# Kernel optimization log

Hardware: AMD Instinct MI355X
Metric: run time of the kernel (lower is better)

Reference implementation:

```python
import jax, jax.numpy as jnp
import numpy as np

RES = 16            # voxel grid resolution (init arg res)
G = RES ** 3        # number of cells = 4096
REG_R = float(np.sqrt(3.0)) / RES  # sqrt(3)/s regularizer radius
B, C, RND, NPTS, H = 16, 64, 2, 16384, 256


def _grid_offsets():
    # util.meshgrid(res): integer grid coords, then ((grid+0.5)/res - 0.5).view(3,-1)
    r = jnp.arange(RES)
    gx, gy, gz = jnp.meshgrid(r, r, r, indexing='ij')
    grid = jnp.stack([gx, gy, gz], 0).reshape(3, -1).astype(jnp.float32)  # [3, G]
    return (grid + 0.5) / RES - 0.5


def _dens_sample(dens, n_points):
    # Deterministic largest-remainder allocation of n_points proportional to density.
    b = dens.shape[0]
    p = dens.reshape(b, -1)
    p = p / jnp.sum(p, axis=-1, keepdims=True)
    scaled = p * n_points                      # [b, G]
    base = jnp.floor(scaled)
    rem = (n_points - jnp.sum(base, axis=-1)).astype(jnp.int32)   # [b]
    frac = scaled - base
    ranks = jnp.argsort(jnp.argsort(-frac, axis=-1), axis=-1)      # rank by fractional part
    return base.astype(jnp.int32) + (ranks < rem[:, None]).astype(jnp.int32)  # [b, G]


def setup_inputs() -> dict:
    key = jax.random.key(0)
    ks = jax.random.split(key, 9)
    cin = C + RND
    f32 = jnp.float32
    return {
        'x': jax.random.normal(ks[0], (B, C, RES, RES, RES), f32),
        'dens': jax.random.uniform(ks[1], (B, RES, RES, RES), f32) + 1e-3,
        'noise': jax.random.uniform(ks[2], (B, RND, NPTS), f32),
        'W1': jax.random.normal(ks[3], (H, cin), f32) * np.float32(1.0 / np.sqrt(cin)),
        'b1': jnp.zeros((H,), f32),
        'W2': jax.random.normal(ks[4], (H, H), f32) * np.float32(1.0 / np.sqrt(H)),
        'b2': jnp.zeros((H,), f32),
        'W3': jax.random.normal(ks[5], (3, H), f32) * np.float32(1.0 / np.sqrt(H)),
        'b3': jnp.zeros((3,), f32),
        'n_points': NPTS,
    }


def reference(x, dens, noise, W1, b1, W2, b2, W3, b3, n_points):
    b, c = x.shape[0], x.shape[1]
    x_flat = x.reshape(b, c, -1)                        # [b, c, G]
    n = _dens_sample(dens, n_points)                    # [b, G] repeat counts, sums to n_points
    # Vectorized replacement for the nonzero()/cat loop: cell i appears n[i] times.
    cell_ids = jnp.arange(G)
    idx = jax.vmap(lambda ni: jnp.repeat(cell_ids, ni, total_repeat_length=n_points))(n)  # [b, n_points]
    x_ind = jnp.take_along_axis(x_flat, idx[:, None, :], axis=2)   # [b, c, n_points]
    o = _grid_offsets()                                 # [3, G]
    gen_off = jnp.transpose(o[:, idx], (1, 0, 2))       # [b, 3, n_points]
    rnd = noise * 2.0 - 1.0                             # uniform in [-1, 1)
    gen_inp = jnp.concatenate([x_ind, rnd], axis=1)     # [b, c+rnd, n_points]
    # pointwise conv1d MLP generator
    h = jax.nn.relu(jnp.einsum('oc,bcn->bon', W1, gen_inp) + b1[:, None])
    h = jax.nn.relu(jnp.einsum('oh,bhn->bon', W2, h) + b2[:, None])
    out = jnp.einsum('oh,bhn->bon', W3, h) + b3[:, None]            # [b, 3, n_points]
    norm = jnp.sqrt(jnp.sum(out * out, axis=1))                      # [b, n_points]
    reg = jnp.maximum(norm - REG_R, 0.0)
    return (out + gen_off, reg)
```

## Files before the change

### kernel.cpp

```cpp
#include <hip/hip_runtime.h>

typedef unsigned long long u64;
typedef _Float16 f16x8 __attribute__((ext_vector_type(8)));
typedef float    f32x4 __attribute__((ext_vector_type(4)));
typedef __fp16   fp16x2 __attribute__((ext_vector_type(2)));

#define G_    4096
#define NPTS  16384

union H8 { _Float16 h[8]; uint4 u; };
union PK2 { fp16x2 h[2]; uint2 u; };
union PK4 { fp16x2 h[4]; uint4 u; };

#define MFMA_(A_,B_,C_) __builtin_amdgcn_mfma_f32_16x16x32_f16((A_),(B_),(C_),0,0,0)


__global__ __launch_bounds__(256) void kP(const float* __restrict__ dens,
                                          int* __restrict__ pc,
                                          const float* __restrict__ W1,
                                          const float* __restrict__ W2,
                                          const float* __restrict__ W3,
                                          _Float16* __restrict__ w1f,
                                          _Float16* __restrict__ w2f,
                                          _Float16* __restrict__ w3f,
                                          float* __restrict__ w1n){
  __shared__ double sred[256];
  __shared__ u64  keys[4096];
  __shared__ int  nvs[4096];
  __shared__ int  binidx[4096];
  __shared__ int  hist[1024];
  __shared__ int  cab[1024];
  __shared__ int  scan[256];
  __shared__ float Sf;
  __shared__ int  remS, BstarS, needS, cntS;
  const int t = threadIdx.x;

  if (blockIdx.x >= 16){
    const int e = (blockIdx.x - 16)*256 + t;
    H8 v;
    if (e < 8192){
      const int RT = e >> 9, kt = (e >> 6) & 7, l = e & 63;
      const int m = RT*16 + (l & 15), k = kt*32 + ((l >> 4) << 3);
      #pragma unroll
      for (int j = 0; j < 8; ++j) v.h[j] = (_Float16)W2[m*256 + k + j];
      *(uint4*)&w2f[e*8] = v.u;
    } else if (e < 10240){
      const int e2 = e - 8192;
      const int RT = e2 >> 7, r2 = e2 & 127, kt = r2 >> 6, l = r2 & 63;
      const int m = RT*16 + (l & 15), k = kt*32 + ((l >> 4) << 3);
      #pragma unroll
      for (int j = 0; j < 8; ++j) v.h[j] = (_Float16)W1[m*66 + k + j];
      *(uint4*)&w1f[e2*8] = v.u;
    } else if (e < 10752){
      const int e3 = e - 10240;
      const int kt = e3 >> 6, l = e3 & 63;
      const int m = l & 15, k = kt*32 + ((l >> 4) << 3);
      #pragma unroll
      for (int j = 0; j < 8; ++j) v.h[j] = (m < 3) ? (_Float16)W3[m*256 + k + j] : (_Float16)0.f;
      *(uint4*)&w3f[e3*8] = v.u;
    } else if (e < 11008){
      const int r = e - 10752;
      w1n[r*2 + 0] = W1[r*66 + 64];
      w1n[r*2 + 1] = W1[r*66 + 65];
    }
    return;
  }

  const int b = blockIdx.x;
  const float* d = dens + b*G_;

  for (int j = t; j < 1024; j += 256) hist[j] = 0;
  if (t == 0) cntS = 0;

  double s = 0.0;
  for (int j = 0; j < 16; ++j) s += (double)d[t + 256*j];
  sred[t] = s; __syncthreads();
  for (int off = 128; off > 0; off >>= 1){
    if (t < off) sred[t] += sred[t + off];
    __syncthreads();
  }
  if (t == 0) Sf = (float)sred[0];
  __syncthreads();
  const float S = Sf;

  int bi[16]; int bs = 0;
  #pragma unroll
  for (int j = 0; j < 16; ++j){
    const int i = t + 256*j;
    const float p  = d[i] / S;
    const float sc = p * 16384.0f;
    const float fl = floorf(sc);
    const float fr = sc - fl;
    bi[j] = (int)fl; bs += bi[j];
    const unsigned fb = __float_as_uint(fr);
    keys[i] = ((u64)fb << 12) | (u64)(4095 - i);
    atomicAdd(&hist[fb >> 20], 1);
  }
  scan[t] = bs; __syncthreads();
  for (int off = 128; off > 0; off >>= 1){
    if (t < off) scan[t] += scan[t + off];
    __syncthreads();
  }
  if (t == 0) remS = 16384 - scan[0];
  __syncthreads();
  const int rem = remS;

  const int h0 = hist[4*t], h1 = hist[4*t+1], h2 = hist[4*t+2], h3 = hist[4*t+3];
  const int gs = h0 + h1 + h2 + h3;
  __syncthreads();
  scan[t] = gs; __syncthreads();
  for (int off = 1; off < 256; off <<= 1){
    const int v2 = (t + off < 256) ? scan[t + off] : 0;
    __syncthreads();
    scan[t] += v2;
    __syncthreads();
  }
  const int sAfter = scan[t] - gs;
  cab[4*t+3] = sAfter;
  cab[4*t+2] = sAfter + h3;
  cab[4*t+1] = sAfter + h3 + h2;
  cab[4*t+0] = sAfter + h3 + h2 + h1;
  if (t == 0){ BstarS = 0x7fffffff; needS = 0; }
  __syncthreads();
  if (rem > 0){
    const int ca[4] = {cab[4*t], cab[4*t+1], cab[4*t+2], cab[4*t+3]};
    const int hh[4] = {h0, h1, h2, h3};
    #pragma unroll
    for (int q = 0; q < 4; ++q)
      if (ca[q] < rem && rem <= ca[q] + hh[q]){ BstarS = 4*t + q; needS = rem - ca[q]; }
  }
  __syncthreads();
  const int Bstar = BstarS, need = needS;

  #pragma unroll
  for (int j = 0; j < 16; ++j){
    const int i = t + 256*j;
    const int bin = (int)(keys[i] >> 32);
    nvs[i] = bi[j] + ((bin > Bstar) ? 1 : 0);
    if (bin == Bstar){ const int pos = atomicAdd(&cntS, 1); binidx[pos] = i; }
  }
  __syncthreads();
  const int cnt = cntS;
  for (int p = t; p < cnt; p += 256){
    const u64 K = keys[binidx[p]];
    int r = 0;
    for (int q = 0; q < cnt; ++q) r += (keys[binidx[q]] > K) ? 1 : 0;
    if (r < need) nvs[binidx[p]] += 1;
  }
  __syncthreads();

  int loc[16]; int ls = 0;
  #pragma unroll
  for (int j = 0; j < 16; ++j){ loc[j] = nvs[t*16 + j]; ls += loc[j]; }
  __syncthreads();
  scan[t] = ls; __syncthreads();
  for (int off = 1; off < 256; off <<= 1){
    const int v2 = (t >= off) ? scan[t - off] : 0;
    __syncthreads();
    scan[t] += v2;
    __syncthreads();
  }
  int off0 = scan[t] - ls;
  int* o = pc + b*NPTS;
  #pragma unroll
  for (int j = 0; j < 16; ++j){
    const int c = t*16 + j;
    for (int r = 0; r < loc[j]; ++r) o[off0++] = c;
  }
}

__global__ __launch_bounds__(256, 3) void kE(
    const float* __restrict__ x, const float* __restrict__ noise,
    const _Float16* __restrict__ w1f, const _Float16* __restrict__ w2f,
    const _Float16* __restrict__ w3f, const float* __restrict__ w1n,
    const float* __restrict__ b1, const float* __restrict__ b2, const float* __restrict__ b3,
    const int* __restrict__ pc, float* __restrict__ out)
{
  __shared__ _Float16 Hb[16384];
  __shared__ int   cells[64];
  __shared__ float rndS[2][64];
  const int b = blockIdx.y, p0 = blockIdx.x*64, tid = threadIdx.x;
  const int w = tid >> 6, lane = tid & 63;

  const int pt_g  = tid >> 2;
  const int cell_g = pc[b*NPTS + p0 + pt_g];
  if (tid < 64) cells[tid] = pc[b*NPTS + p0 + tid];
  if (tid >= 64 && tid < 192){
    const int rr = (tid - 64) >> 6, p = tid & 63;
    rndS[rr][p] = noise[(b*2 + rr)*NPTS + p0 + p]*2.f - 1.f;
  }
  {
    const int koct = tid & 3;
    const int ct = pt_g >> 4, lane2 = (pt_g & 15) + koct*16;
    #pragma unroll
    for (int kt = 0; kt < 2; ++kt){
      const int kbase = kt*32 + koct*8;
      const float* xb = x + ((size_t)(b*64 + kbase))*G_ + cell_g;
      float xv[8];
      #pragma unroll
      for (int j = 0; j < 8; ++j) xv[j] = xb[(size_t)j*G_];
      PK4 v;
      v.h[0] = __builtin_amdgcn_cvt_pkrtz(xv[0], xv[1]);
      v.h[1] = __builtin_amdgcn_cvt_pkrtz(xv[2], xv[3]);
      v.h[2] = __builtin_amdgcn_cvt_pkrtz(xv[4], xv[5]);
      v.h[3] = __builtin_amdgcn_cvt_pkrtz(xv[6], xv[7]);
      *(uint4*)&Hb[((kt*4 + ct)*64 + lane2)*8] = v.u;
    }
  }
  __syncthreads();

  f32x4 acc[4][4];
  const f32x4 zz = {0.f, 0.f, 0.f, 0.f};
  #pragma unroll
  for (int rt = 0; rt < 4; ++rt)
    #pragma unroll
    for (int ct = 0; ct < 4; ++ct) acc[rt][ct] = zz;

  const int wr = w*4;

  __builtin_amdgcn_s_setprio(1);
  #pragma unroll
  for (int kt = 0; kt < 2; ++kt){
    f16x8 B[4];
    #pragma unroll
    for (int ct = 0; ct < 4; ++ct) B[ct] = *(f16x8*)&Hb[((kt*4 + ct)*64 + lane)*8];
    #pragma unroll
    for (int rt = 0; rt < 4; ++rt){
      f16x8 A = *(const f16x8*)&w1f[(((wr + rt)*2 + kt)*64 + lane)*8];
      #pragma unroll
      for (int ct = 0; ct < 4; ++ct)
        acc[rt][ct] = MFMA_(A, B[ct], acc[rt][ct]);
    }
  }
  __builtin_amdgcn_s_setprio(0);

  f16x8 A0[4], A1[4];
  #pragma unroll
  for (int rt = 0; rt < 4; ++rt){
    A0[rt] = *(const f16x8*)&w2f[(((wr + rt)*8 + 0)*64 + lane)*8];
    A1[rt] = *(const f16x8*)&w2f[(((wr + rt)*8 + 1)*64 + lane)*8];
  }

  {
    const int m16 = lane & 15, khi = lane >> 4;
    float rn0[4], rn1[4];
    #pragma unroll
    for (int ct = 0; ct < 4; ++ct){
      rn0[ct] = rndS[0][ct*16 + m16];
      rn1[ct] = rndS[1][ct*16 + m16];
    }
    #pragma unroll
    for (int rt = 0; rt < 4; ++rt){
      const int row0 = w*64 + rt*16 + khi*4;
      const float4 wa = *(const float4*)&w1n[row0*2];
      const float4 wb = *(const float4*)&w1n[row0*2 + 4];
      #pragma unroll
      for (int ct = 0; ct < 4; ++ct){
        acc[rt][ct][0] += wa.x*rn0[ct] + wa.y*rn1[ct];
        acc[rt][ct][1] += wa.z*rn0[ct] + wa.w*rn1[ct];
        acc[rt][ct][2] += wb.x*rn0[ct] + wb.y*rn1[ct];
        acc[rt][ct][3] += wb.z*rn0[ct] + wb.w*rn1[ct];
      }
    }
  }
  __syncthreads();

  #pragma unroll
  for (int rt = 0; rt < 4; ++rt){
    const int row0 = w*64 + rt*16 + ((lane >> 4) << 2);
    const float4 bq = *(const float4*)&b1[row0];
    const int kt2 = row0 >> 5, c16 = (row0 >> 3) & 3, j0 = row0 & 7;
    const int lane2 = (lane & 15) + c16*16;
    #pragma unroll
    for (int ct = 0; ct < 4; ++ct){
      PK2 v;
      v.h[0] = __builtin_amdgcn_cvt_pkrtz(fmaxf(acc[rt][ct][0] + bq.x, 0.f),
                                          fmaxf(acc[rt][ct][1] + bq.y, 0.f));
      v.h[1] = __builtin_amdgcn_cvt_pkrtz(fmaxf(acc[rt][ct][2] + bq.z, 0.f),
                                          fmaxf(acc[rt][ct][3] + bq.w, 0.f));
      *(uint2*)&Hb[((kt2*4 + ct)*64 + lane2)*8 + j0] = v.u;
      acc[rt][ct] = zz;
    }
  }
  __syncthreads();

  __builtin_amdgcn_s_setprio(1);
#define MFMA4(AR, RT) \
    acc[RT][0] = MFMA_(AR, Bv0, acc[RT][0]); \
    acc[RT][1] = MFMA_(AR, Bv1, acc[RT][1]); \
    acc[RT][2] = MFMA_(AR, Bv2, acc[RT][2]); \
    acc[RT][3] = MFMA_(AR, Bv3, acc[RT][3]);
#define L2STEP(KT, ACUR) { \
    f16x8 Bv0 = *(f16x8*)&Hb[(((KT)*4 + 0)*64 + lane)*8]; \
    f16x8 Bv1 = *(f16x8*)&Hb[(((KT)*4 + 1)*64 + lane)*8]; \
    f16x8 Bv2 = *(f16x8*)&Hb[(((KT)*4 + 2)*64 + lane)*8]; \
    f16x8 Bv3 = *(f16x8*)&Hb[(((KT)*4 + 3)*64 + lane)*8]; \
    MFMA4(ACUR[0], 0); \
    if ((KT) + 2 < 8) ACUR[0] = *(const f16x8*)&w2f[(((wr + 0)*8 + (KT) + 2)*64 + lane)*8]; \
    MFMA4(ACUR[1], 1); \
    if ((KT) + 2 < 8) ACUR[1] = *(const f16x8*)&w2f[(((wr + 1)*8 + (KT) + 2)*64 + lane)*8]; \
    MFMA4(ACUR[2], 2); \
    if ((KT) + 2 < 8) ACUR[2] = *(const f16x8*)&w2f[(((wr + 2)*8 + (KT) + 2)*64 + lane)*8]; \
    MFMA4(ACUR[3], 3); \
    if ((KT) + 2 < 8) ACUR[3] = *(const f16x8*)&w2f[(((wr + 3)*8 + (KT) + 2)*64 + lane)*8]; \
  }
  L2STEP(0, A0)
  L2STEP(1, A1)
  L2STEP(2, A0)
  L2STEP(3, A1)
  L2STEP(4, A0)
  L2STEP(5, A1)
  L2STEP(6, A0)
  L2STEP(7, A1)
#undef L2STEP
#undef MFMA4
  __builtin_amdgcn_s_setprio(0);

  f16x8 W3v[8];
  #pragma unroll
  for (int kt = 0; kt < 8; ++kt) W3v[kt] = *(const f16x8*)&w3f[(kt*64 + lane)*8];
  __syncthreads();

  #pragma unroll
  for (int rt = 0; rt < 4; ++rt){
    const int row0 = w*64 + rt*16 + ((lane >> 4) << 2);
    const float4 bq = *(const float4*)&b2[row0];
    const int kt2 = row0 >> 5, c16 = (row0 >> 3) & 3, j0 = row0 & 7;
    const int lane2 = (lane & 15) + c16*16;
    #pragma unroll
    for (int ct = 0; ct < 4; ++ct){
      PK2 v;
      v.h[0] = __builtin_amdgcn_cvt_pkrtz(fmaxf(acc[rt][ct][0] + bq.x, 0.f),
                                          fmaxf(acc[rt][ct][1] + bq.y, 0.f));
      v.h[1] = __builtin_amdgcn_cvt_pkrtz(fmaxf(acc[rt][ct][2] + bq.z, 0.f),
                                          fmaxf(acc[rt][ct][3] + bq.w, 0.f));
      *(uint2*)&Hb[((kt2*4 + ct)*64 + lane2)*8 + j0] = v.u;
    }
  }
  __syncthreads();

  f32x4 a3 = zz;
  __builtin_amdgcn_s_setprio(1);
  #pragma unroll
  for (int kt = 0; kt < 8; ++kt){
    f16x8 B = *(f16x8*)&Hb[((kt*4 + w)*64 + lane)*8];
    a3 = MFMA_(W3v[kt], B, a3);
  }
  __builtin_amdgcn_s_setprio(0);
  if (lane < 16){
    const float ox = a3[0] + b3[0];
    const float oy = a3[1] + b3[1];
    const float oz = a3[2] + b3[2];
    const float nrm = sqrtf(ox*ox + oy*oy + oz*oz);
    const float rg_ = fmaxf(nrm - (float)0.10825317547305482, 0.f);
    const int pt = w*16 + lane;
    const int cell = cells[pt];
    const float fx = ((float)(cell >> 8)        + 0.5f) * 0.0625f - 0.5f;
    const float fy = ((float)((cell >> 4) & 15) + 0.5f) * 0.0625f - 0.5f;
    const float fz = ((float)(cell & 15)        + 0.5f) * 0.0625f - 0.5f;
    const int pidx = p0 + pt;
    out[b*49152 +          pidx] = ox + fx;
    out[b*49152 + 16384 +  pidx] = oy + fy;
    out[b*49152 + 32768 +  pidx] = oz + fz;
    out[786432  + b*16384 + pidx] = rg_;
  }
}

extern "C" void kernel_launch(void* const* d_in, const int* in_sizes, int n_in,
                              void* d_out, int out_size, void* d_ws, size_t ws_size,
                              hipStream_t stream){
  const float* x     = (const float*)d_in[0];
  const float* dens  = (const float*)d_in[1];
  const float* noise = (const float*)d_in[2];
  const float* W1    = (const float*)d_in[3];
  const float* b1    = (const float*)d_in[4];
  const float* W2    = (const float*)d_in[5];
  const float* b2    = (const float*)d_in[6];
  const float* W3    = (const float*)d_in[7];
  const float* b3    = (const float*)d_in[8];

  char* ws = (char*)d_ws;
  int*      pc   = (int*)(ws + 0);
  _Float16* w1f  = (_Float16*)(ws + 1048576);
  _Float16* w2f  = (_Float16*)(ws + 1081344);
  _Float16* w3f  = (_Float16*)(ws + 1212416);
  float*    w1n  = (float*)(ws + 1220608);
  float*    out  = (float*)d_out;

  kP<<<dim3(59),      dim3(256), 0, stream>>>(dens, pc, W1, W2, W3, w1f, w2f, w3f, w1n);
  kE<<<dim3(256, 16), dim3(256), 0, stream>>>(x, noise, w1f, w2f, w3f, w1n,
                                              b1, b2, b3, pc, out);
}
```

Measured before the change: 90.47 us.

## Double points per block to 128 to halve weight loads per point

Each block now processes 128 points instead of 64. Every wave holds 4x8 accumulator tiles, so each W1/W2 fragment loaded from global memory is reused across twice as many point columns, and the grid is halved. The hand-pipelined W2 prefetch macros are replaced by a simple unroll-2 loop. Shared memory doubles to 64KB per block, and the larger accumulator array raises register pressure, so occupancy drops (launch bound lowered from 3 to 2 blocks). The cells cache in shared memory is also dropped in favor of re-reading pc at output time.

```diff
diff --git a/kernel.cpp b/kernel.cpp
--- a/kernel.cpp
+++ b/kernel.cpp
@@ -169,83 +169,72 @@
   }
 }
 
-__global__ __launch_bounds__(256, 3) void kE(
+__global__ __launch_bounds__(256, 2) void kE(
     const float* __restrict__ x, const float* __restrict__ noise,
     const _Float16* __restrict__ w1f, const _Float16* __restrict__ w2f,
     const _Float16* __restrict__ w3f, const float* __restrict__ w1n,
     const float* __restrict__ b1, const float* __restrict__ b2, const float* __restrict__ b3,
     const int* __restrict__ pc, float* __restrict__ out)
 {
-  __shared__ _Float16 Hb[16384];
-  __shared__ int   cells[64];
-  __shared__ float rndS[2][64];
-  const int b = blockIdx.y, p0 = blockIdx.x*64, tid = threadIdx.x;
+  __shared__ _Float16 Hb[32768];
+  __shared__ float rndS[2][128];
+  const int b = blockIdx.y, p0 = blockIdx.x*128, tid = threadIdx.x;
   const int w = tid >> 6, lane = tid & 63;
 
-  const int pt_g  = tid >> 2;
-  const int cell_g = pc[b*NPTS + p0 + pt_g];
-  if (tid < 64) cells[tid] = pc[b*NPTS + p0 + tid];
-  if (tid >= 64 && tid < 192){
-    const int rr = (tid - 64) >> 6, p = tid & 63;
+  {
+    const int rr = tid >> 7, p = tid & 127;
     rndS[rr][p] = noise[(b*2 + rr)*NPTS + p0 + p]*2.f - 1.f;
   }
-  {
-    const int koct = tid & 3;
-    const int ct = pt_g >> 4, lane2 = (pt_g & 15) + koct*16;
-    #pragma unroll
-    for (int kt = 0; kt < 2; ++kt){
-      const int kbase = kt*32 + koct*8;
-      const float* xb = x + ((size_t)(b*64 + kbase))*G_ + cell_g;
-      float xv[8];
-      #pragma unroll
-      for (int j = 0; j < 8; ++j) xv[j] = xb[(size_t)j*G_];
-      PK4 v;
-      v.h[0] = __builtin_amdgcn_cvt_pkrtz(xv[0], xv[1]);
-      v.h[1] = __builtin_amdgcn_cvt_pkrtz(xv[2], xv[3]);
-      v.h[2] = __builtin_amdgcn_cvt_pkrtz(xv[4], xv[5]);
-      v.h[3] = __builtin_amdgcn_cvt_pkrtz(xv[6], xv[7]);
-      *(uint4*)&Hb[((kt*4 + ct)*64 + lane2)*8] = v.u;
-    }
-  }
-  __syncthreads();
-
-  f32x4 acc[4][4];
+  #pragma unroll
+  for (int i = 0; i < 4; ++i){
+    const int e = tid + 256*i;
+    const int pt = e >> 3, koct = e & 7;
+    const int cell = pc[b*NPTS + p0 + pt];
+    const int kt = koct >> 2, k2 = koct & 3;
+    const int lane2 = (pt & 15) + k2*16, ct = pt >> 4;
+    const float* xb = x + ((size_t)(b*64 + koct*8))*G_ + cell;
+    float xv[8];
+    #pragma unroll
+    for (int j = 0; j < 8; ++j) xv[j] = xb[(size_t)j*G_];
+    PK4 v;
+    v.h[0] = __builtin_amdgcn_cvt_pkrtz(xv[0], xv[1]);
+    v.h[1] = __builtin_amdgcn_cvt_pkrtz(xv[2], xv[3]);
+    v.h[2] = __builtin_amdgcn_cvt_pkrtz(xv[4], xv[5]);
+    v.h[3] = __builtin_amdgcn_cvt_pkrtz(xv[6], xv[7]);
+    *(uint4*)&Hb[((kt*8 + ct)*64 + lane2)*8] = v.u;
+  }
+  __syncthreads();
+
+  f32x4 acc[4][8];
   const f32x4 zz = {0.f, 0.f, 0.f, 0.f};
   #pragma unroll
   for (int rt = 0; rt < 4; ++rt)
     #pragma unroll
-    for (int ct = 0; ct < 4; ++ct) acc[rt][ct] = zz;
+    for (int ct = 0; ct < 8; ++ct) acc[rt][ct] = zz;
 
   const int wr = w*4;
 
   __builtin_amdgcn_s_setprio(1);
   #pragma unroll
   for (int kt = 0; kt < 2; ++kt){
-    f16x8 B[4];
-    #pragma unroll
-    for (int ct = 0; ct < 4; ++ct) B[ct] = *(f16x8*)&Hb[((kt*4 + ct)*64 + lane)*8];
+    f16x8 B[8];
+    #pragma unroll
+    for (int ct = 0; ct < 8; ++ct) B[ct] = *(f16x8*)&Hb[((kt*8 + ct)*64 + lane)*8];
     #pragma unroll
     for (int rt = 0; rt < 4; ++rt){
       f16x8 A = *(const f16x8*)&w1f[(((wr + rt)*2 + kt)*64 + lane)*8];
       #pragma unroll
-      for (int ct = 0; ct < 4; ++ct)
+      for (int ct = 0; ct < 8; ++ct)
         acc[rt][ct] = MFMA_(A, B[ct], acc[rt][ct]);
     }
   }
   __builtin_amdgcn_s_setprio(0);
-
-  f16x8 A0[4], A1[4];
-  #pragma unroll
-  for (int rt = 0; rt < 4; ++rt){
-    A0[rt] = *(const f16x8*)&w2f[(((wr + rt)*8 + 0)*64 + lane)*8];
-    A1[rt] = *(const f16x8*)&w2f[(((wr + rt)*8 + 1)*64 + lane)*8];
-  }
 
   {
     const int m16 = lane & 15, khi = lane >> 4;
-    float rn0[4], rn1[4];
-    #pragma unroll
-    for (int ct = 0; ct < 4; ++ct){
+    float rn0[8], rn1[8];
+    #pragma unroll
+    for (int ct = 0; ct < 8; ++ct){
       rn0[ct] = rndS[0][ct*16 + m16];
       rn1[ct] = rndS[1][ct*16 + m16];
     }
@@ -255,7 +244,7 @@
       const float4 wa = *(const float4*)&w1n[row0*2];
       const float4 wb = *(const float4*)&w1n[row0*2 + 4];
       #pragma unroll
-      for (int ct = 0; ct < 4; ++ct){
+      for (int ct = 0; ct < 8; ++ct){
         acc[rt][ct][0] += wa.x*rn0[ct] + wa.y*rn1[ct];
         acc[rt][ct][1] += wa.z*rn0[ct] + wa.w*rn1[ct];
         acc[rt][ct][2] += wb.x*rn0[ct] + wb.y*rn1[ct];
@@ -272,48 +261,32 @@
     const int kt2 = row0 >> 5, c16 = (row0 >> 3) & 3, j0 = row0 & 7;
     const int lane2 = (lane & 15) + c16*16;
     #pragma unroll
-    for (int ct = 0; ct < 4; ++ct){
+    for (int ct = 0; ct < 8; ++ct){
       PK2 v;
       v.h[0] = __builtin_amdgcn_cvt_pkrtz(fmaxf(acc[rt][ct][0] + bq.x, 0.f),
                                           fmaxf(acc[rt][ct][1] + bq.y, 0.f));
       v.h[1] = __builtin_amdgcn_cvt_pkrtz(fmaxf(acc[rt][ct][2] + bq.z, 0.f),
                                           fmaxf(acc[rt][ct][3] + bq.w, 0.f));
-      *(uint2*)&Hb[((kt2*4 + ct)*64 + lane2)*8 + j0] = v.u;
+      *(uint2*)&Hb[((kt2*8 + ct)*64 + lane2)*8 + j0] = v.u;
       acc[rt][ct] = zz;
     }
   }
   __syncthreads();
 
   __builtin_amdgcn_s_setprio(1);
-#define MFMA4(AR, RT) \
-    acc[RT][0] = MFMA_(AR, Bv0, acc[RT][0]); \
-    acc[RT][1] = MFMA_(AR, Bv1, acc[RT][1]); \
-    acc[RT][2] = MFMA_(AR, Bv2, acc[RT][2]); \
-    acc[RT][3] = MFMA_(AR, Bv3, acc[RT][3]);
-#define L2STEP(KT, ACUR) { \
-    f16x8 Bv0 = *(f16x8*)&Hb[(((KT)*4 + 0)*64 + lane)*8]; \
-    f16x8 Bv1 = *(f16x8*)&Hb[(((KT)*4 + 1)*64 + lane)*8]; \
-    f16x8 Bv2 = *(f16x8*)&Hb[(((KT)*4 + 2)*64 + lane)*8]; \
-    f16x8 Bv3 = *(f16x8*)&Hb[(((KT)*4 + 3)*64 + lane)*8]; \
-    MFMA4(ACUR[0], 0); \
-    if ((KT) + 2 < 8) ACUR[0] = *(const f16x8*)&w2f[(((wr + 0)*8 + (KT) + 2)*64 + lane)*8]; \
-    MFMA4(ACUR[1], 1); \
-    if ((KT) + 2 < 8) ACUR[1] = *(const f16x8*)&w2f[(((wr + 1)*8 + (KT) + 2)*64 + lane)*8]; \
-    MFMA4(ACUR[2], 2); \
-    if ((KT) + 2 < 8) ACUR[2] = *(const f16x8*)&w2f[(((wr + 2)*8 + (KT) + 2)*64 + lane)*8]; \
-    MFMA4(ACUR[3], 3); \
-    if ((KT) + 2 < 8) ACUR[3] = *(const f16x8*)&w2f[(((wr + 3)*8 + (KT) + 2)*64 + lane)*8]; \
-  }
-  L2STEP(0, A0)
-  L2STEP(1, A1)
-  L2STEP(2, A0)
-  L2STEP(3, A1)
-  L2STEP(4, A0)
-  L2STEP(5, A1)
-  L2STEP(6, A0)
-  L2STEP(7, A1)
-#undef L2STEP
-#undef MFMA4
+  #pragma unroll 2
+  for (int kt = 0; kt < 8; ++kt){
+    f16x8 B[8];
+    #pragma unroll
+    for (int ct = 0; ct < 8; ++ct) B[ct] = *(f16x8*)&Hb[((kt*8 + ct)*64 + lane)*8];
+    #pragma unroll
+    for (int rt = 0; rt < 4; ++rt){
+      f16x8 A = *(const f16x8*)&w2f[(((wr + rt)*8 + kt)*64 + lane)*8];
+      #pragma unroll
+      for (int ct = 0; ct < 8; ++ct)
+        acc[rt][ct] = MFMA_(A, B[ct], acc[rt][ct]);
+    }
+  }
   __builtin_amdgcn_s_setprio(0);
 
   f16x8 W3v[8];
@@ -328,41 +301,46 @@
     const int kt2 = row0 >> 5, c16 = (row0 >> 3) & 3, j0 = row0 & 7;
     const int lane2 = (lane & 15) + c16*16;
     #pragma unroll
-    for (int ct = 0; ct < 4; ++ct){
+    for (int ct = 0; ct < 8; ++ct){
       PK2 v;
       v.h[0] = __builtin_amdgcn_cvt_pkrtz(fmaxf(acc[rt][ct][0] + bq.x, 0.f),
                                           fmaxf(acc[rt][ct][1] + bq.y, 0.f));
       v.h[1] = __builtin_amdgcn_cvt_pkrtz(fmaxf(acc[rt][ct][2] + bq.z, 0.f),
                                           fmaxf(acc[rt][ct][3] + bq.w, 0.f));
-      *(uint2*)&Hb[((kt2*4 + ct)*64 + lane2)*8 + j0] = v.u;
-    }
-  }
-  __syncthreads();
-
-  f32x4 a3 = zz;
+      *(uint2*)&Hb[((kt2*8 + ct)*64 + lane2)*8 + j0] = v.u;
+    }
+  }
+  __syncthreads();
+
+  f32x4 a3[2] = {zz, zz};
   __builtin_amdgcn_s_setprio(1);
   #pragma unroll
   for (int kt = 0; kt < 8; ++kt){
-    f16x8 B = *(f16x8*)&Hb[((kt*4 + w)*64 + lane)*8];
-    a3 = MFMA_(W3v[kt], B, a3);
+    f16x8 B0 = *(f16x8*)&Hb[((kt*8 + w*2 + 0)*64 + lane)*8];
+    f16x8 B1 = *(f16x8*)&Hb[((kt*8 + w*2 + 1)*64 + lane)*8];
+    a3[0] = MFMA_(W3v[kt], B0, a3[0]);
+    a3[1] = MFMA_(W3v[kt], B1, a3[1]);
   }
   __builtin_amdgcn_s_setprio(0);
   if (lane < 16){
-    const float ox = a3[0] + b3[0];
-    const float oy = a3[1] + b3[1];
-    const float oz = a3[2] + b3[2];
-    const float nrm = sqrtf(ox*ox + oy*oy + oz*oz);
-    const float rg_ = fmaxf(nrm - (float)0.10825317547305482, 0.f);
-    const int pt = w*16 + lane;
-    const int cell = cells[pt];
-    const float fx = ((float)(cell >> 8)        + 0.5f) * 0.0625f - 0.5f;
-    const float fy = ((float)((cell >> 4) & 15) + 0.5f) * 0.0625f - 0.5f;
-    const float fz = ((float)(cell & 15)        + 0.5f) * 0.0625f - 0.5f;
-    const int pidx = p0 + pt;
-    out[b*49152 +          pidx] = ox + fx;
-    out[b*49152 + 16384 +  pidx] = oy + fy;
-    out[b*49152 + 32768 +  pidx] = oz + fz;
-    out[786432  + b*16384 + pidx] = rg_;
+    #pragma unroll
+    for (int q = 0; q < 2; ++q){
+      const float ox = a3[q][0] + b3[0];
+      const float oy = a3[q][1] + b3[1];
+      const float oz = a3[q][2] + b3[2];
+      const float nrm = sqrtf(ox*ox + oy*oy + oz*oz);
+      const float rg_ = fmaxf(nrm - (float)0.10825317547305482, 0.f);
+      const int pt = (w*2 + q)*16 + lane;
+      const int pidx = p0 + pt;
+      const int cell = pc[b*NPTS + pidx];
+      const float fx = ((float)(cell >> 8)        + 0.5f) * 0.0625f - 0.5f;
+      const float fy = ((float)((cell >> 4) & 15) + 0.5f) * 0.0625f - 0.5f;
+      const float fz = ((float)(cell & 15)        + 0.5f) * 0.0625f - 0.5f;
+      out[b*49152 +          pidx] = ox + fx;
+      out[b*49152 + 16384 +  pidx] = oy + fy;
+      out[b*49152 + 32768 +  pidx] = oz + fz;
+      out[786432  + b*16384 + pidx] = rg_;
+    }
   }
 }
 
@@ -388,6 +366,6 @@
   float*    out  = (float*)d_out;
 
   kP<<<dim3(59),      dim3(256), 0, stream>>>(dens, pc, W1, W2, W3, w1f, w2f, w3f, w1n);
-  kE<<<dim3(256, 16), dim3(256), 0, stream>>>(x, noise, w1f, w2f, w3f, w1n,
+  kE<<<dim3(128, 16), dim3(256), 0, stream>>>(x, noise, w1f, w2f, w3f, w1n,
                                               b1, b2, b3, pc, out);
 }
```

New measurement: 89.59 us. About the same (-1.0%).
